# Kernel optimization log

Measured on AMD Instinct MI355X. Metric: run time of the kernel, lower is better.

The kernel has to match this reference:

```python
import jax, jax.numpy as jnp
import numpy as np
from jax import lax

H = 4096          # hidden_size
NH = 32           # num_attention_heads
NKV = 8           # num_key_value_heads
HD = H // NH      # head_dim = 128
CACHE = 2048      # state_length (kv cache length)
POS = 1024        # current decode position
THETA = 10000.0


def _rope_tables():
    inv_freq = 1.0 / (THETA ** (np.arange(0, HD, 2, dtype=np.float32) / HD))
    t = np.arange(CACHE * 2, dtype=np.float32)
    freqs = np.einsum('i,j->ij', t, inv_freq)          # [2*CACHE, HD/2]
    emb = np.concatenate([freqs, freqs], axis=-1)      # [2*CACHE, HD]
    return (jnp.asarray(np.cos(emb)[None]),            # [1, 2*CACHE, HD]
            jnp.asarray(np.sin(emb)[None]))


def setup_inputs() -> dict:
    key = jax.random.key(0)
    ks = jax.random.split(key, 8)
    cos_cached, sin_cached = _rope_tables()
    # additive causal mask for decode: positions <= current_pos visible
    mask = jnp.where(jnp.arange(CACHE) <= POS, 0.0, -1e9).astype(jnp.float32)
    return {
        'hidden_states': jax.random.normal(ks[0], (1, 1, H), dtype=jnp.float32),
        'attention_mask': mask.reshape(1, 1, 1, CACHE),
        'key_cache': jax.random.normal(ks[1], (1, NKV, CACHE, HD), dtype=jnp.float32),
        'value_cache': jax.random.normal(ks[2], (1, NKV, CACHE, HD), dtype=jnp.float32),
        'q_w': jax.random.normal(ks[3], (NH * HD, H), dtype=jnp.float32) * 0.02,
        'k_w': jax.random.normal(ks[4], (NKV * HD, H), dtype=jnp.float32) * 0.02,
        'v_w': jax.random.normal(ks[5], (NKV * HD, H), dtype=jnp.float32) * 0.02,
        'o_w': jax.random.normal(ks[6], (H, NH * HD), dtype=jnp.float32) * 0.02,
        'cos_cached': cos_cached,
        'sin_cached': sin_cached,
        'position_ids': jnp.full((1, 1), POS, dtype=jnp.int32),
        'current_pos': POS,
    }


def _rotate(x, cos, sin):
    # x: [1, nheads, 1, HD]; cos/sin: [1, 1, 1, HD] (full dim, halves identical)
    half = x.shape[-1] // 2
    x1, x2 = x[..., :half], x[..., half:]
    c, s = cos[..., :half], sin[..., :half]
    return jnp.concatenate([x1 * c - x2 * s, x2 * c + x1 * s], axis=-1)


def reference(hidden_states, attention_mask, key_cache, value_cache,
              q_w, k_w, v_w, o_w, cos_cached, sin_cached,
              position_ids, current_pos):
    # --- QKV projections (1x1 Conv2d == linear) on the single decode token ---
    x = hidden_states[:, 0, :]                           # [1, H]
    q = (x @ q_w.T).reshape(1, NH, 1, HD)
    k = (x @ k_w.T).reshape(1, NKV, 1, HD)
    v = (x @ v_w.T).reshape(1, NKV, 1, HD)

    # --- inline RoPE at current_pos ---
    cos_t = lax.dynamic_slice(cos_cached, (0, current_pos, 0), (1, 1, HD))[:, None]  # [1,1,1,HD]
    sin_t = lax.dynamic_slice(sin_cached, (0, current_pos, 0), (1, 1, HD))[:, None]
    q = _rotate(q, cos_t, sin_t)
    k = _rotate(k, cos_t, sin_t)

    # --- KV-cache append ---
    key_cache = lax.dynamic_update_slice(key_cache, k, (0, 0, current_pos, 0))
    value_cache = lax.dynamic_update_slice(value_cache, v, (0, 0, current_pos, 0))

    # --- GQA scaled dot-product attention over the cache ---
    groups = NH // NKV
    K = jnp.repeat(key_cache, groups, axis=1)            # [1, NH, CACHE, HD]
    V = jnp.repeat(value_cache, groups, axis=1)
    scale = 1.0 / np.sqrt(HD)
    scores = jnp.einsum('bhqd,bhkd->bhqk', q, K) * scale + attention_mask
    attn = jax.nn.softmax(scores, axis=-1)
    ctx = jnp.einsum('bhqk,bhkd->bhqd', attn, V)         # [1, NH, 1, HD]

    # --- output projection ---
    ctx = ctx.transpose(0, 2, 1, 3).reshape(1, 1, NH * HD)
    return jnp.einsum('bsd,od->bso', ctx, o_w)           # [1, 1, H]
```

## Files before the change

### kernel.cpp

```cpp
#include <hip/hip_runtime.h>
#include <math.h>

#define H      4096
#define NH     32
#define NKV    8
#define HD     128
#define CACHE  2048
#define GROUPS (NH / NKV)
#define CHUNK  32
#define NSPL   (CACHE / CHUNK)
#define KSTR   132
#define SCALE  0.08838834764831845f

#define QOFF 0
#define KOFF 4096
#define VOFF 5120
#define POFF 6144
#define PSTRIDE 132
#define CTXOFF (POFF + NH * NSPL * PSTRIDE)

__global__ __launch_bounds__(256) void qkv_gemv(
    const float* __restrict__ x,
    const float* __restrict__ qw, const float* __restrict__ kw,
    const float* __restrict__ vw, float* __restrict__ ws) {
  __shared__ float xs[H];
  const int t = threadIdx.x;
  {
    const float4* xr = (const float4*)x;
    float4* xsv = (float4*)xs;
#pragma unroll
    for (int i = 0; i < 4; ++i) xsv[i * 256 + t] = xr[i * 256 + t];
  }
  __syncthreads();

  const int wave = t >> 6;
  const int lane = t & 63;
  const int row  = blockIdx.x * 4 + wave;

  const float* w;
  float* outp;
  int r;
  if (row < 4096)      { w = qw; r = row;        outp = ws + QOFF; }
  else if (row < 5120) { w = kw; r = row - 4096; outp = ws + KOFF; }
  else                 { w = vw; r = row - 5120; outp = ws + VOFF; }

  const float4* wr = (const float4*)(w + (size_t)r * H);
  float4 a[16];
#pragma unroll
  for (int j = 0; j < 16; ++j) a[j] = wr[j * 64 + lane];

  float sum = 0.f;
#pragma unroll
  for (int j = 0; j < 16; ++j) {
    const float4 b = *(const float4*)&xs[(j * 64 + lane) * 4];
    sum = fmaf(a[j].x, b.x, sum);
    sum = fmaf(a[j].y, b.y, sum);
    sum = fmaf(a[j].z, b.z, sum);
    sum = fmaf(a[j].w, b.w, sum);
  }
#pragma unroll
  for (int off = 32; off > 0; off >>= 1) sum += __shfl_xor(sum, off);
  if (lane == 0) outp[r] = sum;
}

__global__ __launch_bounds__(256) void attn_split(
    const float* __restrict__ kcache, const float* __restrict__ vcache,
    const float* __restrict__ cosc, const float* __restrict__ sinc,
    const int* __restrict__ curp, float* __restrict__ ws) {
  const int kh    = blockIdx.x;
  const int split = blockIdx.y;
  const int cur   = curp[0];
  const int total = cur + 1;
  const int p0    = split * CHUNK;
  if (p0 >= total) return;

  __shared__ float Ks[CHUNK * KSTR];
  __shared__ float Vs[CHUNK * KSTR];
  __shared__ float q_s[GROUPS * HD];
  __shared__ float es[GROUPS][CHUNK];

  const int t = threadIdx.x;

  {
    const int r4 = t >> 5;
    const int c4 = (t & 31) * 4;
    const float* kb = kcache + (size_t)kh * CACHE * HD;
    const float* vb = vcache + (size_t)kh * CACHE * HD;
#pragma unroll
    for (int rr = 0; rr < CHUNK; rr += 8) {
      const int row = rr + r4;
      const int p   = min(p0 + row, cur);
      if (p0 + row != cur) {
        float4 kv = *(const float4*)(kb + (size_t)p * HD + c4);
        float4 vv = *(const float4*)(vb + (size_t)p * HD + c4);
        *(float4*)&Ks[row * KSTR + c4] = kv;
        *(float4*)&Vs[row * KSTR + c4] = vv;
      }
    }
  }
#pragma unroll
  for (int i = 0; i < 2; ++i) {
    const int idx = t + i * 256;
    const int qh = idx >> 7, d = idx & 127;
    const int h = kh * GROUPS + qh;
    const float c  = cosc[(size_t)cur * HD + d];
    const float s  = sinc[(size_t)cur * HD + d];
    const float x1 = ws[QOFF + h * HD + d];
    const float x2 = (d < HD / 2) ? -ws[QOFF + h * HD + d + HD / 2]
                                  :  ws[QOFF + h * HD + d - HD / 2];
    q_s[qh * HD + d] = x1 * c + x2 * s;
  }
  if (cur >= p0 && cur < p0 + CHUNK) {
    const int row = cur - p0;
    if (t < HD) {
      const int d = t;
      const float c  = cosc[(size_t)cur * HD + d];
      const float s  = sinc[(size_t)cur * HD + d];
      const float k1 = ws[KOFF + kh * HD + d];
      const float k2 = (d < HD / 2) ? -ws[KOFF + kh * HD + d + HD / 2]
                                    :  ws[KOFF + kh * HD + d - HD / 2];
      Ks[row * KSTR + d] = k1 * c + k2 * s;
    } else if (t < 2 * HD) {
      const int d = t - HD;
      Vs[row * KSTR + d] = ws[VOFF + kh * HD + d];
    }
  }
  __syncthreads();

  if (t < 128) {
    const int qh = t >> 5, pos = t & 31;
    float4 a = make_float4(0.f, 0.f, 0.f, 0.f);
#pragma unroll
    for (int j = 0; j < HD / 4; ++j) {
      float4 kv = *(const float4*)&Ks[pos * KSTR + j * 4];
      float4 qv = *(const float4*)&q_s[qh * HD + j * 4];
      a.x += kv.x * qv.x; a.y += kv.y * qv.y;
      a.z += kv.z * qv.z; a.w += kv.w * qv.w;
    }
    float s = (a.x + a.y + a.z + a.w) * SCALE;
    const bool valid = (p0 + pos) < total;
    s = valid ? s : -INFINITY;
    float m = s;
#pragma unroll
    for (int off = 16; off > 0; off >>= 1) m = fmaxf(m, __shfl_xor(m, off));
    const float e = valid ? __expf(s - m) : 0.f;
    float l = e;
#pragma unroll
    for (int off = 16; off > 0; off >>= 1) l += __shfl_xor(l, off);
    es[qh][pos] = e;
    if (pos == 0) {
      float* part = ws + POFF + (size_t)((kh * GROUPS + qh) * NSPL + split) * PSTRIDE;
      part[0] = m; part[1] = l;
    }
  }
  __syncthreads();

  {
    const int qh = t >> 6;
    const int d0 = (t & 63) * 2;
    float2 acc = make_float2(0.f, 0.f);
#pragma unroll
    for (int pos = 0; pos < CHUNK; ++pos) {
      const float w = es[qh][pos];
      const float2 vv = *(const float2*)&Vs[pos * KSTR + d0];
      acc.x += w * vv.x; acc.y += w * vv.y;
    }
    float* part = ws + POFF + (size_t)((kh * GROUPS + qh) * NSPL + split) * PSTRIDE;
    part[4 + d0]     = acc.x;
    part[4 + d0 + 1] = acc.y;
  }
}

__global__ __launch_bounds__(128) void attn_combine(
    const int* __restrict__ curp, float* __restrict__ ws) {
  const int h = blockIdx.x;
  const int t = threadIdx.x;
  const int total = curp[0] + 1;
  const int nspl = (total + CHUNK - 1) / CHUNK;
  __shared__ float wsh[64];
  __shared__ float Lsh;

  if (t < 64) {
    float mt = -INFINITY, lt = 0.f;
    if (t < nspl) {
      const float* part = ws + POFF + (size_t)(h * NSPL + t) * PSTRIDE;
      mt = part[0]; lt = part[1];
    }
    float M = mt;
#pragma unroll
    for (int off = 32; off > 0; off >>= 1) M = fmaxf(M, __shfl_xor(M, off));
    const float w = (t < nspl) ? __expf(mt - M) : 0.f;
    float lw = lt * w;
#pragma unroll
    for (int off = 32; off > 0; off >>= 1) lw += __shfl_xor(lw, off);
    wsh[t] = w;
    if (t == 0) Lsh = lw;
  }
  __syncthreads();

  const float Linv = 1.f / Lsh;
  float acc = 0.f;
#pragma unroll 8
  for (int i = 0; i < nspl; ++i)
    acc += wsh[i] * ws[POFF + (size_t)(h * NSPL + i) * PSTRIDE + 4 + t];
  ws[CTXOFF + h * HD + t] = acc * Linv;
}

__global__ __launch_bounds__(256) void o_gemv(
    const float* __restrict__ ow, const float* __restrict__ ws,
    float* __restrict__ out) {
  __shared__ float xs[H];
  const int t = threadIdx.x;
  {
    const float4* xr = (const float4*)(ws + CTXOFF);
    float4* xsv = (float4*)xs;
#pragma unroll
    for (int i = 0; i < 4; ++i) xsv[i * 256 + t] = xr[i * 256 + t];
  }
  __syncthreads();

  const int wave = t >> 6;
  const int lane = t & 63;
  const int row  = blockIdx.x * 4 + wave;

  const float4* wr = (const float4*)(ow + (size_t)row * H);
  float4 a[16];
#pragma unroll
  for (int j = 0; j < 16; ++j) a[j] = wr[j * 64 + lane];

  float sum = 0.f;
#pragma unroll
  for (int j = 0; j < 16; ++j) {
    const float4 b = *(const float4*)&xs[(j * 64 + lane) * 4];
    sum = fmaf(a[j].x, b.x, sum);
    sum = fmaf(a[j].y, b.y, sum);
    sum = fmaf(a[j].z, b.z, sum);
    sum = fmaf(a[j].w, b.w, sum);
  }
#pragma unroll
  for (int off = 32; off > 0; off >>= 1) sum += __shfl_xor(sum, off);
  if (lane == 0) out[row] = sum;
}

extern "C" void kernel_launch(void* const* d_in, const int* in_sizes, int n_in,
                              void* d_out, int out_size, void* d_ws, size_t ws_size,
                              hipStream_t stream) {
  const float* hs   = (const float*)d_in[0];
  const float* kc   = (const float*)d_in[2];
  const float* vc   = (const float*)d_in[3];
  const float* qw   = (const float*)d_in[4];
  const float* kw   = (const float*)d_in[5];
  const float* vw   = (const float*)d_in[6];
  const float* ow   = (const float*)d_in[7];
  const float* cosc = (const float*)d_in[8];
  const float* sinc = (const float*)d_in[9];
  const int*   cur  = (const int*)d_in[11];
  float* ws  = (float*)d_ws;
  float* out = (float*)d_out;

  qkv_gemv<<<1536, 256, 0, stream>>>(hs, qw, kw, vw, ws);
  attn_split<<<dim3(NKV, NSPL), 256, 0, stream>>>(kc, vc, cosc, sinc, cur, ws);
  attn_combine<<<NH, 128, 0, stream>>>(cur, ws);
  o_gemv<<<1024, 256, 0, stream>>>(ow, ws, out);
}
```

Measured before the change: 41.91 us.

## Fuse split-KV combine into attention kernel via last-block atomic counter

Removes the separate attn_combine launch. Each split block increments a per-KV-head atomic counter after a threadfence, and the last block to finish for that head merges all partial softmax results for its four query heads and writes the context. The counter is zeroed by the QKV GEMV kernel. This saves one kernel launch and its dependency gap, but the final merge is serialized onto one block per KV head.

Measured after the change: 52.30 us. 24.8% more time.

```diff
diff --git a/kernel.cpp b/kernel.cpp
--- a/kernel.cpp
+++ b/kernel.cpp
@@ -18,6 +18,7 @@
 #define POFF 6144
 #define PSTRIDE 132
 #define CTXOFF (POFF + NH * NSPL * PSTRIDE)
+#define CNTOFF (CTXOFF + 4096)
 
 __global__ __launch_bounds__(256) void qkv_gemv(
     const float* __restrict__ x,
@@ -25,6 +26,7 @@
     const float* __restrict__ vw, float* __restrict__ ws) {
   __shared__ float xs[H];
   const int t = threadIdx.x;
+  if (blockIdx.x == 0 && t < NKV) ((int*)(ws + CNTOFF))[t] = 0;
   {
     const float4* xr = (const float4*)x;
     float4* xsv = (float4*)xs;
@@ -73,11 +75,15 @@
   const int total = cur + 1;
   const int p0    = split * CHUNK;
   if (p0 >= total) return;
+  const int nactive = (total + CHUNK - 1) / CHUNK;
 
   __shared__ float Ks[CHUNK * KSTR];
   __shared__ float Vs[CHUNK * KSTR];
   __shared__ float q_s[GROUPS * HD];
   __shared__ float es[GROUPS][CHUNK];
+  __shared__ float cw[GROUPS][64];
+  __shared__ float cLinv[GROUPS];
+  __shared__ int   lastflag;
 
   const int t = threadIdx.x;
 
@@ -169,41 +175,45 @@
     part[4 + d0]     = acc.x;
     part[4 + d0 + 1] = acc.y;
   }
-}
-
-__global__ __launch_bounds__(128) void attn_combine(
-    const int* __restrict__ curp, float* __restrict__ ws) {
-  const int h = blockIdx.x;
-  const int t = threadIdx.x;
-  const int total = curp[0] + 1;
-  const int nspl = (total + CHUNK - 1) / CHUNK;
-  __shared__ float wsh[64];
-  __shared__ float Lsh;
-
-  if (t < 64) {
+
+  if (t == 0) {
+    __threadfence();
+    int* cnt = (int*)(ws + CNTOFF);
+    const int old = __hip_atomic_fetch_add(&cnt[kh], 1, __ATOMIC_ACQ_REL,
+                                           __HIP_MEMORY_SCOPE_AGENT);
+    lastflag = (old == nactive - 1);
+  }
+  __syncthreads();
+  if (!lastflag) return;
+
+  {
+    const int qh   = t >> 6;
+    const int lane = t & 63;
+    const float* pb = ws + POFF + (size_t)((kh * GROUPS + qh) * NSPL) * PSTRIDE;
     float mt = -INFINITY, lt = 0.f;
-    if (t < nspl) {
-      const float* part = ws + POFF + (size_t)(h * NSPL + t) * PSTRIDE;
-      mt = part[0]; lt = part[1];
-    }
+    if (lane < nactive) { mt = pb[lane * PSTRIDE]; lt = pb[lane * PSTRIDE + 1]; }
     float M = mt;
 #pragma unroll
     for (int off = 32; off > 0; off >>= 1) M = fmaxf(M, __shfl_xor(M, off));
-    const float w = (t < nspl) ? __expf(mt - M) : 0.f;
-    float lw = lt * w;
+    const float wgt = (lane < nactive) ? __expf(mt - M) : 0.f;
+    float lw = lt * wgt;
 #pragma unroll
     for (int off = 32; off > 0; off >>= 1) lw += __shfl_xor(lw, off);
-    wsh[t] = w;
-    if (t == 0) Lsh = lw;
-  }
-  __syncthreads();
-
-  const float Linv = 1.f / Lsh;
-  float acc = 0.f;
-#pragma unroll 8
-  for (int i = 0; i < nspl; ++i)
-    acc += wsh[i] * ws[POFF + (size_t)(h * NSPL + i) * PSTRIDE + 4 + t];
-  ws[CTXOFF + h * HD + t] = acc * Linv;
+    cw[qh][lane] = wgt;
+    if (lane == 0) cLinv[qh] = 1.f / lw;
+  }
+  __syncthreads();
+#pragma unroll
+  for (int i = 0; i < 2; ++i) {
+    const int idx = t + i * 256;
+    const int hh  = idx >> 7;
+    const int d   = idx & 127;
+    const float* pb = ws + POFF + (size_t)((kh * GROUPS + hh) * NSPL) * PSTRIDE;
+    float acc = 0.f;
+    for (int s = 0; s < nactive; ++s)
+      acc += cw[hh][s] * pb[s * PSTRIDE + 4 + d];
+    ws[CTXOFF + (kh * GROUPS + hh) * HD + d] = acc * cLinv[hh];
+  }
 }
 
 __global__ __launch_bounds__(256) void o_gemv(
@@ -260,6 +270,5 @@
 
   qkv_gemv<<<1536, 256, 0, stream>>>(hs, qw, kw, vw, ws);
   attn_split<<<dim3(NKV, NSPL), 256, 0, stream>>>(kc, vc, cosc, sinc, cur, ws);
-  attn_combine<<<NH, 128, 0, stream>>>(cur, ws);
   o_gemv<<<1024, 256, 0, stream>>>(ow, ws, out);
 }
```
